# Kernel tuning notes

Hardware: AMD Instinct MI355X
Metric: run time of the kernel (lower is better)

The kernel has to match this reference:

```python
import jax, jax.numpy as jnp
import numpy as np

B, LSEQ = 128, 4096
NUM_EXPERTS, TOP_K = 8, 2
OUT_SEQ = 256
AUX_FACTOR = 0.01


def _conv1d(x, w, b, stride, pad):
    # x: [B, Cin, L], w: [Cout, Cin, K]
    y = jax.lax.conv_general_dilated(x, w, (stride,), [(pad, pad)],
                                     dimension_numbers=('NCH', 'OIH', 'NCH'))
    return y + b[None, :, None]


def setup_inputs() -> dict:
    key = jax.random.key(0)
    ks = jax.random.split(key, 9)
    s = 0.05
    return {
        'x': jax.random.normal(ks[0], (B, LSEQ), jnp.float32),
        # gating conv net (in_channels=2 -> 32 -> 64, kernel 5, padding same)
        'g_w1': jax.random.normal(ks[1], (32, 2, 5), jnp.float32) * s,
        'g_b1': jnp.zeros((32,), jnp.float32),
        'g_w2': jax.random.normal(ks[2], (64, 32, 5), jnp.float32) * s,
        'g_b2': jnp.zeros((64,), jnp.float32),
        # gating MLP (64 -> 128 -> num_experts)
        'm_w1': jax.random.normal(ks[3], (128, 64), jnp.float32) * s,
        'm_b1': jnp.zeros((128,), jnp.float32),
        'm_w2': jax.random.normal(ks[4], (NUM_EXPERTS, 128), jnp.float32) * s,
        'm_b2': jnp.zeros((NUM_EXPERTS,), jnp.float32),
        # expert CNN stacks, stacked over experts (same shapes per expert)
        'ew1': jax.random.normal(ks[5], (NUM_EXPERTS, 64, 2, 7), jnp.float32) * s,
        'eb1': jnp.zeros((NUM_EXPERTS, 64), jnp.float32),
        'ew2': jax.random.normal(ks[6], (NUM_EXPERTS, 128, 64, 5), jnp.float32) * s,
        'eb2': jnp.zeros((NUM_EXPERTS, 128), jnp.float32),
        'ew3': jax.random.normal(ks[7], (NUM_EXPERTS, 128, 128, 3), jnp.float32) * s,
        'eb3': jnp.zeros((NUM_EXPERTS, 128), jnp.float32),
    }


def reference(x, g_w1, g_b1, g_w2, g_b2, m_w1, m_b1, m_w2, m_b2,
              ew1, eb1, ew2, eb2, ew3, eb3):
    b, lseq = x.shape
    # periodic Hann window (torch.hann_window default)
    win = 0.5 * (1.0 - jnp.cos(2.0 * jnp.pi * jnp.arange(lseq, dtype=x.dtype) / lseq))
    xf = jnp.fft.rfft(x * win, norm='ortho')
    fft = jnp.stack([xf.real, xf.imag], axis=1)  # [B, 2, Lf]

    # gating: conv -> relu -> conv -> relu -> global avg pool -> MLP (dropout in eval)
    h = jax.nn.relu(_conv1d(fft, g_w1, g_b1, 1, 2))
    h = jax.nn.relu(_conv1d(h, g_w2, g_b2, 1, 2))
    pooled = h.mean(-1)  # [B, 64]
    logits = jax.nn.relu(pooled @ m_w1.T + m_b1) @ m_w2.T + m_b2  # [B, E]
    rw = jax.nn.softmax(logits, axis=1)
    aux = AUX_FACTOR * NUM_EXPERTS * (rw.mean(0) * logits.mean(0)).sum()

    tw, ti = jax.lax.top_k(rw, TOP_K)  # [B, K]
    tw = tw / tw.sum(-1, keepdims=True)

    # Each (token, k) pair routes fft[b] to expert ti[b,k]; compute each expert
    # densely over the batch and gather (same math as masked dispatch/combine).
    def expert(w1, b1, w2, b2, w3, b3):
        e = jax.nn.relu(_conv1d(fft, w1, b1, 2, 3))
        e = jax.nn.relu(_conv1d(e, w2, b2, 2, 2))
        e = jax.nn.relu(_conv1d(e, w3, b3, 1, 1))
        return e

    out_stack = jax.vmap(expert)(ew1, eb1, ew2, eb2, ew3, eb3)  # [E, B, C, L]
    sel = out_stack[ti, jnp.arange(b)[:, None]]                 # [B, K, C, L]
    final = (sel * tw[:, :, None, None]).sum(1)                 # [B, C, L]

    # adaptive max pool 1d to OUT_SEQ (PyTorch window rule)
    L = final.shape[-1]
    starts = np.floor(np.arange(OUT_SEQ) * L / OUT_SEQ).astype(np.int32)
    ends = np.ceil((np.arange(OUT_SEQ) + 1) * L / OUT_SEQ).astype(np.int32)
    maxw = int((ends - starts).max())
    raw = starts[:, None] + np.arange(maxw)[None, :]
    valid = jnp.asarray(raw < ends[:, None])
    idx = np.minimum(raw, L - 1)
    g = final[..., idx]  # [B, C, OUT_SEQ, maxw]
    resized = jnp.max(jnp.where(valid, g, -jnp.inf), axis=-1)
    return (resized, aux)
```

## Files before the change

kernel.cpp:

```cpp
#include <hip/hip_runtime.h>

#define NFREQ 2049
#define L1LEN 1025
#define L2LEN 513

typedef short v8s  __attribute__((ext_vector_type(8)));
typedef float v16f __attribute__((ext_vector_type(16)));
typedef unsigned short ushort_t;
typedef unsigned int uint_t;

#define OFF_FFT     0ull
#define OFF_TWID    524544ull
#define OFF_PTW     526592ull
#define OFF_WIN     530944ull
#define OFF_PART    535040ull
#define OFF_TW      1075712ull
#define OFF_TI      1075968ull
#define OFF_SRWLOG  1076224ull
#define OFF_W2HF    1076480ull
#define OFF_W2LF    1081600ull
#define OFF_W2F     1086720ull
#define OFF_W3F     1250560ull
#define OFF_A       1447168ull
#define OFF_E2U     9852160ull

#define E2U_K_STRIDE 8404992

__device__ __forceinline__ float relu_f(float x) { return fmaxf(x, 0.0f); }
__device__ __forceinline__ int   rfl_i(int v)   { return __builtin_amdgcn_readfirstlane(v); }
__device__ __forceinline__ float rfl_f(float v) { return __uint_as_float((unsigned)__builtin_amdgcn_readfirstlane((int)__float_as_uint(v))); }
__device__ __forceinline__ ushort_t f2bf(float x) {
    unsigned u = __float_as_uint(x);
    unsigned r = (u + 0x7FFFu + ((u >> 16) & 1u)) >> 16;
    return (ushort_t)r;
}
__device__ __forceinline__ float bf2f(ushort_t h) { return __uint_as_float(((unsigned)h) << 16); }

__global__ void init_kernel(float* SRWLOG, float* TWID, float* PTW, float* WIN,
                            ushort_t* W2HF, ushort_t* W2LF, ushort_t* W2F, ushort_t* W3F,
                            const float* g_w2, const float* ew2, const float* ew3) {
    const float PI = 3.14159265358979323846f;
    int tid = blockIdx.x * blockDim.x + threadIdx.x;
    int stride = gridDim.x * blockDim.x;
    for (int i = tid; i < 16; i += stride) SRWLOG[i] = 0.0f;
    for (int j = tid; j < 1024; j += stride) {
        float a = PI * (float)j / 1024.0f;
        TWID[2 * j] = cosf(a);
        TWID[2 * j + 1] = -sinf(a);
    }
    for (int k = tid; k < 2049; k += stride) {
        float a = PI * (float)k / 2048.0f;
        PTW[2 * k] = cosf(a);
        PTW[2 * k + 1] = sinf(a);
    }
    for (int n = tid; n < 4096; n += stride) {
        WIN[n] = 0.5f * (1.0f - cosf(2.0f * PI * (float)n / 4096.0f));
    }
    for (int i = tid; i < 10240; i += stride) {
        int j = i & 7;
        int lane = (i >> 3) & 63;
        int ks = (i >> 9) & 1;
        int tile = (i >> 10) & 1;
        int t = i >> 11;
        int o = tile * 32 + (lane & 31);
        int c = ks * 16 + (lane >> 5) * 8 + j;
        float w = g_w2[o * 160 + c * 5 + t];
        ushort_t h = f2bf(w);
        W2HF[i] = h;
        W2LF[i] = f2bf(w - bf2f(h));
    }
    for (int i = tid; i < 327680; i += stride) {
        int j = i & 7;
        int lane = (i >> 3) & 63;
        int ks = (i >> 9) & 3;
        int w = (i >> 11) & 3;
        int t = (i >> 13) % 5;
        int e = i / 40960;
        int o = w * 32 + (lane & 31);
        int c = ks * 16 + (lane >> 5) * 8 + j;
        W2F[i] = f2bf(ew2[((e * 128 + o) * 64 + c) * 5 + t]);
    }
    for (int i = tid; i < 393216; i += stride) {
        int j = i & 7;
        int lane = (i >> 3) & 63;
        int ks = (i >> 9) & 7;
        int w = (i >> 12) & 3;
        int t = (i >> 14) % 3;
        int e = i / 49152;
        int o = w * 32 + (lane & 31);
        int c = ks * 16 + (lane >> 5) * 8 + j;
        W3F[i] = f2bf(ew3[((e * 128 + o) * 128 + c) * 3 + t]);
    }
}

__global__ __launch_bounds__(1024) void fft_kernel(const float* __restrict__ x,
                                                   const float* __restrict__ TWID,
                                                   const float* __restrict__ PTW,
                                                   const float* __restrict__ WIN,
                                                   float* __restrict__ FFT) {
    __shared__ float re[2048];
    __shared__ float im[2048];
    int b = blockIdx.x, t = threadIdx.x;
    const float* xb = x + b * 4096;
    for (int i = t; i < 2048; i += 1024) {
        int j = (int)(__brev((unsigned)i) >> 21);
        re[i] = xb[2 * j] * WIN[2 * j];
        im[i] = xb[2 * j + 1] * WIN[2 * j + 1];
    }
    for (int s = 1; s <= 11; ++s) {
        __syncthreads();
        int half = 1 << (s - 1);
        int shift = 11 - s;
        int bf = t;
        {
            int grp = bf >> (s - 1);
            int pos = bf & (half - 1);
            int i1 = (grp << s) + pos;
            int i2 = i1 + half;
            int j = pos << shift;
            float wr = TWID[2 * j], wi = TWID[2 * j + 1];
            float ar = re[i2], ai = im[i2];
            float tr = wr * ar - wi * ai;
            float ti = wr * ai + wi * ar;
            float br = re[i1], bi = im[i1];
            re[i2] = br - tr; im[i2] = bi - ti;
            re[i1] = br + tr; im[i1] = bi + ti;
        }
    }
    __syncthreads();
    const float scale = 1.0f / 64.0f;
    for (int k = t; k <= 2048; k += 1024) {
        int k1 = k & 2047;
        int k2 = (2048 - k) & 2047;
        float zr = re[k1], zi = im[k1];
        float yr = re[k2], yi = im[k2];
        float Er = 0.5f * (zr + yr), Ei = 0.5f * (zi - yi);
        float Or = 0.5f * (zi + yi), Oi = 0.5f * (yr - zr);
        float c2 = PTW[2 * k], s3 = PTW[2 * k + 1];
        FFT[b * 4098 + k]        = (Er + c2 * Or + s3 * Oi) * scale;
        FFT[b * 4098 + 2049 + k] = (Ei + c2 * Oi - s3 * Or) * scale;
    }
}

__global__ __launch_bounds__(256) void g12_kernel(const float* __restrict__ FFT,
                                                  const float* __restrict__ g_w1, const float* __restrict__ g_b1,
                                                  const ushort_t* __restrict__ W2HF, const ushort_t* __restrict__ W2LF,
                                                  const float* __restrict__ g_b2,
                                                  float* __restrict__ PART) {
    __shared__ float fx[2][72];
    __shared__ float w1S[320];
    __shared__ float b1S[32];
    __shared__ __align__(16) char un[17408];
    ushort_t (*xh)[40] = (ushort_t (*)[40])un;
    ushort_t (*xl)[40] = (ushort_t (*)[40])(un + 5440);
    float (*red)[68]  = (float (*)[68])un;
    int b = blockIdx.y;
    int q0 = blockIdx.x * 64;
    int t = threadIdx.x;
    for (int i = t; i < 352; i += 256) {
        if (i < 320) w1S[i] = g_w1[i];
        else b1S[i - 320] = g_b1[i - 320];
    }
    {
        const float* fb = FFT + b * 4098;
        for (int i = t; i < 144; i += 256) {
            int ch = i / 72, u = i % 72;
            int P = q0 - 4 + u;
            fx[ch][u] = (P >= 0 && P < NFREQ) ? fb[ch * NFREQ + P] : 0.0f;
        }
    }
    __syncthreads();
    {
        int c = t & 31;
        float bias = b1S[c];
        float wr[10];
        #pragma unroll
        for (int j = 0; j < 10; ++j) wr[j] = w1S[c * 10 + j];
        for (int i = t; i < 544; i += 256) {
            int g4 = (i >> 5) << 2;
            float4 x00 = *(const float4*)&fx[0][g4];
            float4 x01 = *(const float4*)&fx[0][g4 + 4];
            float4 x10 = *(const float4*)&fx[1][g4];
            float4 x11 = *(const float4*)&fx[1][g4 + 4];
            float xa[8] = {x00.x, x00.y, x00.z, x00.w, x01.x, x01.y, x01.z, x01.w};
            float xb_[8] = {x10.x, x10.y, x10.z, x10.w, x11.x, x11.y, x11.z, x11.w};
            #pragma unroll
            for (int rr = 0; rr < 4; ++rr) {
                int row = g4 + rr;
                int pos = q0 - 2 + row;
                ushort_t h = 0, l = 0;
                if (pos >= 0 && pos < NFREQ) {
                    float a = bias;
                    #pragma unroll
                    for (int tt = 0; tt < 5; ++tt) a = fmaf(xa[rr + tt], wr[tt], a);
                    #pragma unroll
                    for (int tt = 0; tt < 5; ++tt) a = fmaf(xb_[rr + tt], wr[5 + tt], a);
                    a = relu_f(a);
                    h = f2bf(a);
                    l = f2bf(a - bf2f(h));
                }
                xh[row][c] = h;
                xl[row][c] = l;
            }
        }
    }
    __syncthreads();
    int lane = t & 63;
    int w = rfl_i(t >> 6);
    int tile = w & 1;
    int qh = w >> 1;
    int n = lane & 31;
    int kg = lane >> 5;
    v16f acc;
    #pragma unroll
    for (int i = 0; i < 16; ++i) acc[i] = 0.0f;
    #pragma unroll
    for (int t5 = 0; t5 < 5; ++t5) {
        int row = qh * 32 + n + t5;
        #pragma unroll
        for (int ks = 0; ks < 2; ++ks) {
            int c0 = ks * 16 + kg * 8;
            v8s Ah = *(const v8s*)(W2HF + (((t5 * 2 + tile) * 2 + ks) << 9) + lane * 8);
            v8s Al = *(const v8s*)(W2LF + (((t5 * 2 + tile) * 2 + ks) << 9) + lane * 8);
            v8s Bh = *(const v8s*)&xh[row][c0];
            v8s Bl = *(const v8s*)&xl[row][c0];
            acc = __builtin_amdgcn_mfma_f32_32x32x16_bf16(Ah, Bh, acc, 0, 0, 0);
            acc = __builtin_amdgcn_mfma_f32_32x32x16_bf16(Ah, Bl, acc, 0, 0, 0);
            acc = __builtin_amdgcn_mfma_f32_32x32x16_bf16(Al, Bh, acc, 0, 0, 0);
        }
    }
    __syncthreads();
    {
        int q = q0 + qh * 32 + n;
        bool valid = (q < NFREQ);
        #pragma unroll
        for (int r = 0; r < 16; ++r) {
            int m = (r & 3) + 8 * (r >> 2) + 4 * kg;
            int o = tile * 32 + m;
            red[o][qh * 32 + n] = valid ? relu_f(acc[r] + g_b2[o]) : 0.0f;
        }
    }
    __syncthreads();
    {
        int o = t >> 2;
        int qq = t & 3;
        float s = 0.0f;
        #pragma unroll
        for (int u = 0; u < 4; ++u) {
            float4 vv = *(const float4*)&red[o][qq * 16 + u * 4];
            s += vv.x + vv.y + vv.z + vv.w;
        }
        s += __shfl_xor(s, 1, 64);
        s += __shfl_xor(s, 2, 64);
        if (qq == 0) PART[(b * 64 + o) * 66 + blockIdx.x] = s;
    }
}

__global__ __launch_bounds__(128) void mlp_kernel(const float* __restrict__ PART,
                                                  const float* __restrict__ m_w1, const float* __restrict__ m_b1,
                                                  const float* __restrict__ m_w2, const float* __restrict__ m_b2,
                                                  float* TW, int* TI, float* SRWLOG) {
    __shared__ float pooledS[64];
    __shared__ float hid[128];
    __shared__ float lgS[8];
    __shared__ float rwS[8];
    int b = blockIdx.x, t = threadIdx.x;
    if (t < 64) {
        float s = 0.0f;
        const float* pp = PART + (b * 64 + t) * 66;
        for (int blk = 0; blk < 33; ++blk) s += pp[blk];
        pooledS[t] = s;
    }
    __syncthreads();
    const float inv = 1.0f / 2049.0f;
    {
        float h = m_b1[t];
        for (int c = 0; c < 64; ++c)
            h = fmaf(pooledS[c] * inv, m_w1[t * 64 + c], h);
        hid[t] = relu_f(h);
    }
    __syncthreads();
    if (t < 8) {
        float lg = m_b2[t];
        for (int j = 0; j < 128; ++j) lg = fmaf(hid[j], m_w2[t * 128 + j], lg);
        lgS[t] = lg;
    }
    __syncthreads();
    if (t == 0) {
        float mx = lgS[0];
        for (int e = 1; e < 8; ++e) mx = fmaxf(mx, lgS[e]);
        float s = 0.0f, ex[8];
        for (int e = 0; e < 8; ++e) { ex[e] = expf(lgS[e] - mx); s += ex[e]; }
        for (int e = 0; e < 8; ++e) rwS[e] = ex[e] / s;
        int i1 = 0;
        for (int e = 1; e < 8; ++e) if (rwS[e] > rwS[i1]) i1 = e;
        int i2 = (i1 == 0) ? 1 : 0;
        for (int e = 0; e < 8; ++e) if (e != i1 && rwS[e] > rwS[i2]) i2 = e;
        float t0 = rwS[i1], t1 = rwS[i2], sm = t0 + t1;
        TW[b * 2] = t0 / sm; TW[b * 2 + 1] = t1 / sm;
        TI[b * 2] = i1; TI[b * 2 + 1] = i2;
    }
    __syncthreads();
    if (t < 8) {
        atomicAdd(&SRWLOG[t], rwS[t]);
        atomicAdd(&SRWLOG[8 + t], lgS[t]);
    }
}

__global__ __launch_bounds__(256) void e12_kernel(const float* __restrict__ FFT,
                                                  const float* __restrict__ ew1, const float* __restrict__ eb1,
                                                  const ushort_t* __restrict__ W2F, const float* __restrict__ eb2,
                                                  const int* __restrict__ TI, ushort_t* __restrict__ E2u) {
    __shared__ float fxs[2][272];
    __shared__ __align__(16) char sm2[19008];
    ushort_t (*xe)[72] = (ushort_t (*)[72])sm2;
    ushort_t (*xo)[72] = (ushort_t (*)[72])(sm2 + 9504);
    ushort_t (*oT)[136] = (ushort_t (*)[136])sm2;
    int b = blockIdx.x;
    int k = blockIdx.z;
    int q0 = blockIdx.y * 64;
    int t = threadIdx.x;
    int e = rfl_i(TI[b * 2 + k]);
    {
        const float* fb = FFT + b * 4098;
        for (int i = t; i < 544; i += 256) {
            int ch = i / 272, off = i - ch * 272;
            int P = 4 * q0 - 7 + off;
            fxs[ch][off] = (P >= 0 && P < NFREQ) ? fb[ch * NFREQ + P] : 0.0f;
        }
    }
    int c = t & 63;
    float w1r[14];
    #pragma unroll
    for (int j = 0; j < 14; ++j) w1r[j] = ew1[(e * 64 + c) * 14 + j];
    float b1r = eb1[e * 64 + c];
    __syncthreads();
    {
        int g0 = t >> 6;
        for (int r = g0; r < 132; r += 4) {
            int p = 2 * q0 - 2 + r;
            ushort_t val = 0;
            if (p >= 0 && p < L1LEN) {
                float a = b1r;
                #pragma unroll
                for (int tt = 0; tt < 7; ++tt) a = fmaf(fxs[0][2 * r + tt], w1r[tt], a);
                #pragma unroll
                for (int tt = 0; tt < 7; ++tt) a = fmaf(fxs[1][2 * r + tt], w1r[7 + tt], a);
                val = f2bf(relu_f(a));
            }
            if (r & 1) xo[r >> 1][c] = val;
            else       xe[r >> 1][c] = val;
        }
    }
    __syncthreads();
    int lane = t & 63;
    int w = rfl_i(t >> 6);
    int n = lane & 31;
    int kg = lane >> 5;
    v16f acc0, acc1;
    #pragma unroll
    for (int i = 0; i < 16; ++i) { acc0[i] = 0.0f; acc1[i] = 0.0f; }
    #pragma unroll
    for (int t5 = 0; t5 < 5; ++t5) {
        int roff = t5 >> 1;
        const ushort_t (*sel)[72] = (t5 & 1) ? xo : xe;
        const ushort_t* wfrag = W2F + ((((e * 5 + t5) * 4 + w) * 4) << 9) + lane * 8;
        #pragma unroll
        for (int ks = 0; ks < 4; ++ks) {
            int c0 = ks * 16 + kg * 8;
            v8s a = *(const v8s*)(wfrag + (ks << 9));
            v8s b0 = *(const v8s*)&sel[n + roff][c0];
            v8s b1 = *(const v8s*)&sel[n + 32 + roff][c0];
            acc0 = __builtin_amdgcn_mfma_f32_32x32x16_bf16(a, b0, acc0, 0, 0, 0);
            acc1 = __builtin_amdgcn_mfma_f32_32x32x16_bf16(a, b1, acc1, 0, 0, 0);
        }
    }
    __syncthreads();
    #pragma unroll
    for (int g = 0; g < 4; ++g) {
        int ob = w * 32 + 8 * g + 4 * kg;
        uint_t p00 = (uint_t)f2bf(relu_f(acc0[4 * g + 0] + eb2[e * 128 + ob + 0]))
                   | ((uint_t)f2bf(relu_f(acc0[4 * g + 1] + eb2[e * 128 + ob + 1])) << 16);
        uint_t p01 = (uint_t)f2bf(relu_f(acc0[4 * g + 2] + eb2[e * 128 + ob + 2]))
                   | ((uint_t)f2bf(relu_f(acc0[4 * g + 3] + eb2[e * 128 + ob + 3])) << 16);
        uint_t p10 = (uint_t)f2bf(relu_f(acc1[4 * g + 0] + eb2[e * 128 + ob + 0]))
                   | ((uint_t)f2bf(relu_f(acc1[4 * g + 1] + eb2[e * 128 + ob + 1])) << 16);
        uint_t p11 = (uint_t)f2bf(relu_f(acc1[4 * g + 2] + eb2[e * 128 + ob + 2]))
                   | ((uint_t)f2bf(relu_f(acc1[4 * g + 3] + eb2[e * 128 + ob + 3])) << 16);
        uint2 v0; v0.x = p00; v0.y = p01;
        uint2 v1; v1.x = p10; v1.y = p11;
        *(uint2*)&oT[n][ob]      = v0;
        *(uint2*)&oT[32 + n][ob] = v1;
    }
    __syncthreads();
    ushort_t* E2k = E2u + (size_t)k * E2U_K_STRIDE;
    for (int i = t; i < 64 * 16; i += 256) {
        int qq = i >> 4, c8 = (i & 15) * 8;
        int q = q0 + qq;
        if (q < L2LEN)
            *(uint4*)(E2k + ((size_t)b * L2LEN + q) * 128 + c8) = *(const uint4*)&oT[qq][c8];
    }
}

__global__ __launch_bounds__(256) void e3_kernel(const ushort_t* __restrict__ E2u,
                                                 const ushort_t* __restrict__ W3F, const float* __restrict__ eb3,
                                                 const int* __restrict__ TI, const float* __restrict__ TW,
                                                 float* __restrict__ FINAL) {
    __shared__ __align__(16) ushort_t xT[2][66][136];
    int b = blockIdx.x;
    int q0 = blockIdx.y * 64;
    int t = threadIdx.x;
    int lane = t & 63;
    int ow = rfl_i(t >> 6);
    int n = lane & 31;
    int kg = lane >> 5;
    int e0  = rfl_i(TI[b * 2]);
    int e1_ = rfl_i(TI[b * 2 + 1]);
    float wk0 = rfl_f(TW[b * 2]);
    float wk1 = rfl_f(TW[b * 2 + 1]);
    for (int i = t; i < 1056; i += 256) {
        int row = i >> 4, c8 = (i & 15) * 8;
        int pos = q0 - 1 + row;
        uint4 v; v.x = 0u; v.y = 0u; v.z = 0u; v.w = 0u;
        if (pos >= 0 && pos < L2LEN)
            v = *(const uint4*)(E2u + ((size_t)b * L2LEN + pos) * 128 + c8);
        *(uint4*)&xT[0][row][c8] = v;
    }
    __syncthreads();
    uint4 st[5];
    #pragma unroll
    for (int j = 0; j < 5; ++j) {
        int i = t + j * 256;
        uint4 v; v.x = 0u; v.y = 0u; v.z = 0u; v.w = 0u;
        if (i < 1056) {
            int row = i >> 4, c8 = (i & 15) * 8;
            int pos = q0 - 1 + row;
            if (pos >= 0 && pos < L2LEN)
                v = *(const uint4*)(E2u + (size_t)E2U_K_STRIDE + ((size_t)b * L2LEN + pos) * 128 + c8);
        }
        st[j] = v;
    }
    float res0[16], res1[16];
    #pragma unroll
    for (int i = 0; i < 16; ++i) { res0[i] = 0.0f; res1[i] = 0.0f; }
    {
        v16f a0, a1;
        #pragma unroll
        for (int i = 0; i < 16; ++i) { a0[i] = 0.0f; a1[i] = 0.0f; }
        #pragma unroll
        for (int t3 = 0; t3 < 3; ++t3) {
            const ushort_t* wfrag = W3F + ((((e0 * 3 + t3) * 4 + ow) * 8) << 9) + lane * 8;
            #pragma unroll
            for (int ks = 0; ks < 8; ++ks) {
                int c0 = ks * 16 + kg * 8;
                v8s a = *(const v8s*)(wfrag + (ks << 9));
                v8s b0 = *(const v8s*)&xT[0][n + t3][c0];
                v8s b1 = *(const v8s*)&xT[0][32 + n + t3][c0];
                a0 = __builtin_amdgcn_mfma_f32_32x32x16_bf16(a, b0, a0, 0, 0, 0);
                a1 = __builtin_amdgcn_mfma_f32_32x32x16_bf16(a, b1, a1, 0, 0, 0);
            }
        }
        #pragma unroll
        for (int r = 0; r < 16; ++r) {
            int m = (r & 3) + 8 * (r >> 2) + 4 * kg;
            float bias = eb3[e0 * 128 + ow * 32 + m];
            res0[r] += relu_f(a0[r] + bias) * wk0;
            res1[r] += relu_f(a1[r] + bias) * wk0;
        }
    }
    #pragma unroll
    for (int j = 0; j < 5; ++j) {
        int i = t + j * 256;
        if (i < 1056) {
            int row = i >> 4, c8 = (i & 15) * 8;
            *(uint4*)&xT[1][row][c8] = st[j];
        }
    }
    __syncthreads();
    {
        v16f a0, a1;
        #pragma unroll
        for (int i = 0; i < 16; ++i) { a0[i] = 0.0f; a1[i] = 0.0f; }
        #pragma unroll
        for (int t3 = 0; t3 < 3; ++t3) {
            const ushort_t* wfrag = W3F + ((((e1_ * 3 + t3) * 4 + ow) * 8) << 9) + lane * 8;
            #pragma unroll
            for (int ks = 0; ks < 8; ++ks) {
                int c0 = ks * 16 + kg * 8;
                v8s a = *(const v8s*)(wfrag + (ks << 9));
                v8s b0 = *(const v8s*)&xT[1][n + t3][c0];
                v8s b1 = *(const v8s*)&xT[1][32 + n + t3][c0];
                a0 = __builtin_amdgcn_mfma_f32_32x32x16_bf16(a, b0, a0, 0, 0, 0);
                a1 = __builtin_amdgcn_mfma_f32_32x32x16_bf16(a, b1, a1, 0, 0, 0);
            }
        }
        #pragma unroll
        for (int r = 0; r < 16; ++r) {
            int m = (r & 3) + 8 * (r >> 2) + 4 * kg;
            float bias = eb3[e1_ * 128 + ow * 32 + m];
            res0[r] += relu_f(a0[r] + bias) * wk1;
            res1[r] += relu_f(a1[r] + bias) * wk1;
        }
    }
    float* Fb = FINAL + (size_t)b * 128 * 513;
    int qA = q0 + n;
    int qB = q0 + 32 + n;
    #pragma unroll
    for (int r = 0; r < 16; ++r) {
        int m = (r & 3) + 8 * (r >> 2) + 4 * kg;
        int o = ow * 32 + m;
        if (qA < L2LEN) Fb[o * 513 + qA] = res0[r];
        if (qB < L2LEN) Fb[o * 513 + qB] = res1[r];
    }
}

__global__ __launch_bounds__(256) void pool_kernel(const float* __restrict__ FINAL,
                                                   const float* __restrict__ SRWLOG,
                                                   float* __restrict__ out) {
    if (blockIdx.x == 0 && threadIdx.x == 0) {
        float a = 0.0f;
        for (int e = 0; e < 8; ++e)
            a += (SRWLOG[e] / 128.0f) * (SRWLOG[8 + e] / 128.0f);
        out[4194304] = 0.01f * 8.0f * a;
    }
    int idx = blockIdx.x * 256 + threadIdx.x;
    int j = idx & 255;
    int row = idx >> 8;
    const float* f = FINAL + (size_t)row * 513;
    int s = (513 * j) >> 8;
    int e_ = (513 * (j + 1) + 255) >> 8;
    float m = f[s];
    for (int p = s + 1; p < e_; ++p) m = fmaxf(m, f[p]);
    out[idx] = m;
}

extern "C" void kernel_launch(void* const* d_in, const int* in_sizes, int n_in,
                              void* d_out, int out_size, void* d_ws, size_t ws_size,
                              hipStream_t stream) {
    const float* x    = (const float*)d_in[0];
    const float* g_w1 = (const float*)d_in[1];
    const float* g_b1 = (const float*)d_in[2];
    const float* g_w2 = (const float*)d_in[3];
    const float* g_b2 = (const float*)d_in[4];
    const float* m_w1 = (const float*)d_in[5];
    const float* m_b1 = (const float*)d_in[6];
    const float* m_w2 = (const float*)d_in[7];
    const float* m_b2 = (const float*)d_in[8];
    const float* ew1  = (const float*)d_in[9];
    const float* eb1  = (const float*)d_in[10];
    const float* ew2  = (const float*)d_in[11];
    const float* eb2  = (const float*)d_in[12];
    const float* ew3  = (const float*)d_in[13];
    const float* eb3  = (const float*)d_in[14];

    float* ws     = (float*)d_ws;
    float* FFT    = ws + OFF_FFT;
    float* TWID   = ws + OFF_TWID;
    float* PTW    = ws + OFF_PTW;
    float* WIN    = ws + OFF_WIN;
    float* PART   = ws + OFF_PART;
    float* TW     = ws + OFF_TW;
    int*   TI     = (int*)(ws + OFF_TI);
    float* SRWLOG = ws + OFF_SRWLOG;
    ushort_t* W2HF = (ushort_t*)(ws + OFF_W2HF);
    ushort_t* W2LF = (ushort_t*)(ws + OFF_W2LF);
    ushort_t* W2F  = (ushort_t*)(ws + OFF_W2F);
    ushort_t* W3F  = (ushort_t*)(ws + OFF_W3F);
    float* FINAL  = ws + OFF_A;
    ushort_t* E2u = (ushort_t*)(ws + OFF_E2U);
    float* out    = (float*)d_out;

    init_kernel<<<512, 256, 0, stream>>>(SRWLOG, TWID, PTW, WIN, W2HF, W2LF, W2F, W3F, g_w2, ew2, ew3);
    fft_kernel<<<128, 1024, 0, stream>>>(x, TWID, PTW, WIN, FFT);
    g12_kernel<<<dim3(33, 128), 256, 0, stream>>>(FFT, g_w1, g_b1, W2HF, W2LF, g_b2, PART);
    mlp_kernel<<<128, 128, 0, stream>>>(PART, m_w1, m_b1, m_w2, m_b2, TW, TI, SRWLOG);
    e12_kernel<<<dim3(128, 9, 2), 256, 0, stream>>>(FFT, ew1, eb1, W2F, eb2, TI, E2u);
    e3_kernel<<<dim3(128, 9), 256, 0, stream>>>(E2u, W3F, eb3, TI, TW, FINAL);
    pool_kernel<<<16384, 256, 0, stream>>>(FINAL, SRWLOG, out);
}
```

Measured before the change: 216.9 us.

## Drop ninth tile of expert conv kernels; compute last position with scalar tail

The expert conv kernels previously launched nine position tiles of 64, where the ninth covered only position 512 of 513. The grid now uses eight tiles, and the last block computes that single output position with a scalar fp32 loop over the original weights, using halo rows already in shared memory. Bounds checks on stores are removed. The pool kernel becomes grid-stride with fewer blocks. This trades a mostly idle tile of MFMA work for a serial per-thread dot product in one block, which can lengthen that block's critical path.

After: 232.1 us. 7.0% more time.

```diff
diff --git a/kernel.cpp b/kernel.cpp
--- a/kernel.cpp
+++ b/kernel.cpp
@@ -309,6 +309,7 @@
 
 __global__ __launch_bounds__(256) void e12_kernel(const float* __restrict__ FFT,
                                                   const float* __restrict__ ew1, const float* __restrict__ eb1,
+                                                  const float* __restrict__ ew2,
                                                   const ushort_t* __restrict__ W2F, const float* __restrict__ eb2,
                                                   const int* __restrict__ TI, ushort_t* __restrict__ E2u) {
     __shared__ float fxs[2][272];
@@ -375,6 +376,21 @@
             acc1 = __builtin_amdgcn_mfma_f32_32x32x16_bf16(a, b1, acc1, 0, 0, 0);
         }
     }
+    if (blockIdx.y == 7 && t < 128) {
+        int ob = t;
+        float a = eb2[e * 128 + ob];
+        const float* w2row = ew2 + (size_t)(e * 128 + ob) * 64 * 5;
+        const ushort_t* r0 = xe[64];
+        const ushort_t* r1 = xo[64];
+        const ushort_t* r2 = xe[65];
+        for (int cc = 0; cc < 64; ++cc) {
+            const float* wc = w2row + cc * 5;
+            a = fmaf(bf2f(r0[cc]), wc[0], a);
+            a = fmaf(bf2f(r1[cc]), wc[1], a);
+            a = fmaf(bf2f(r2[cc]), wc[2], a);
+        }
+        E2u[(size_t)k * E2U_K_STRIDE + ((size_t)b * L2LEN + 512) * 128 + ob] = f2bf(relu_f(a));
+    }
     __syncthreads();
     #pragma unroll
     for (int g = 0; g < 4; ++g) {
@@ -397,13 +413,13 @@
     for (int i = t; i < 64 * 16; i += 256) {
         int qq = i >> 4, c8 = (i & 15) * 8;
         int q = q0 + qq;
-        if (q < L2LEN)
-            *(uint4*)(E2k + ((size_t)b * L2LEN + q) * 128 + c8) = *(const uint4*)&oT[qq][c8];
+        *(uint4*)(E2k + ((size_t)b * L2LEN + q) * 128 + c8) = *(const uint4*)&oT[qq][c8];
     }
 }
 
 __global__ __launch_bounds__(256) void e3_kernel(const ushort_t* __restrict__ E2u,
                                                  const ushort_t* __restrict__ W3F, const float* __restrict__ eb3,
+                                                 const float* __restrict__ ew3,
                                                  const int* __restrict__ TI, const float* __restrict__ TW,
                                                  float* __restrict__ FINAL) {
     __shared__ __align__(16) ushort_t xT[2][66][136];
@@ -502,6 +518,26 @@
             res1[r] += relu_f(a1[r] + bias) * wk1;
         }
     }
+    if (blockIdx.y == 7 && t < 128) {
+        int o = t;
+        float r512 = 0.0f;
+        #pragma unroll
+        for (int k = 0; k < 2; ++k) {
+            int e = (k == 0) ? e0 : e1_;
+            float wk = (k == 0) ? wk0 : wk1;
+            float a = eb3[e * 128 + o];
+            const float* w3row = ew3 + (size_t)(e * 128 + o) * 128 * 3;
+            const ushort_t* er0 = xT[k][64];
+            const ushort_t* er1 = xT[k][65];
+            for (int cc = 0; cc < 128; ++cc) {
+                const float* wc = w3row + cc * 3;
+                a = fmaf(bf2f(er0[cc]), wc[0], a);
+                a = fmaf(bf2f(er1[cc]), wc[1], a);
+            }
+            r512 += relu_f(a) * wk;
+        }
+        FINAL[(size_t)b * 128 * 513 + (size_t)o * 513 + 512] = r512;
+    }
     float* Fb = FINAL + (size_t)b * 128 * 513;
     int qA = q0 + n;
     int qB = q0 + 32 + n;
@@ -509,8 +545,8 @@
     for (int r = 0; r < 16; ++r) {
         int m = (r & 3) + 8 * (r >> 2) + 4 * kg;
         int o = ow * 32 + m;
-        if (qA < L2LEN) Fb[o * 513 + qA] = res0[r];
-        if (qB < L2LEN) Fb[o * 513 + qB] = res1[r];
+        Fb[o * 513 + qA] = res0[r];
+        Fb[o * 513 + qB] = res1[r];
     }
 }
 
@@ -523,15 +559,16 @@
             a += (SRWLOG[e] / 128.0f) * (SRWLOG[8 + e] / 128.0f);
         out[4194304] = 0.01f * 8.0f * a;
     }
-    int idx = blockIdx.x * 256 + threadIdx.x;
-    int j = idx & 255;
-    int row = idx >> 8;
-    const float* f = FINAL + (size_t)row * 513;
-    int s = (513 * j) >> 8;
-    int e_ = (513 * (j + 1) + 255) >> 8;
-    float m = f[s];
-    for (int p = s + 1; p < e_; ++p) m = fmaxf(m, f[p]);
-    out[idx] = m;
+    for (int idx = blockIdx.x * 256 + threadIdx.x; idx < 4194304; idx += 2048 * 256) {
+        int j = idx & 255;
+        int row = idx >> 8;
+        const float* f = FINAL + (size_t)row * 513;
+        int s = (513 * j) >> 8;
+        int e_ = (513 * (j + 1) + 255) >> 8;
+        float m = f[s];
+        for (int p = s + 1; p < e_; ++p) m = fmaxf(m, f[p]);
+        out[idx] = m;
+    }
 }
 
 extern "C" void kernel_launch(void* const* d_in, const int* in_sizes, int n_in,
@@ -574,7 +611,7 @@
     fft_kernel<<<128, 1024, 0, stream>>>(x, TWID, PTW, WIN, FFT);
     g12_kernel<<<dim3(33, 128), 256, 0, stream>>>(FFT, g_w1, g_b1, W2HF, W2LF, g_b2, PART);
     mlp_kernel<<<128, 128, 0, stream>>>(PART, m_w1, m_b1, m_w2, m_b2, TW, TI, SRWLOG);
-    e12_kernel<<<dim3(128, 9, 2), 256, 0, stream>>>(FFT, ew1, eb1, W2F, eb2, TI, E2u);
-    e3_kernel<<<dim3(128, 9), 256, 0, stream>>>(E2u, W3F, eb3, TI, TW, FINAL);
-    pool_kernel<<<16384, 256, 0, stream>>>(FINAL, SRWLOG, out);
-}
+    e12_kernel<<<dim3(128, 8, 2), 256, 0, stream>>>(FFT, ew1, eb1, ew2, W2F, eb2, TI, E2u);
+    e3_kernel<<<dim3(128, 8), 256, 0, stream>>>(E2u, W3F, eb3, ew3, TI, TW, FINAL);
+    pool_kernel<<<2048, 256, 0, stream>>>(FINAL, SRWLOG, out);
+}
```
